# Kernel tuning notes

Measured on AMD Instinct MI355X. Metric: run time of the kernel, lower is better.

## Reference

```python
import jax, jax.numpy as jnp
import numpy as np

SEQ_LEN = 4096
DIM_HALF = 2048  # x last dim = 2 * DIM_HALF
DIM_OUT = 1024
LN_EPS = 1e-5


def setup_inputs() -> dict:
    key = jax.random.key(0)
    k1, k2, k3 = jax.random.split(key, 3)
    x = jax.random.normal(k1, (SEQ_LEN, 2 * DIM_HALF), dtype=jnp.float32)
    ln_scale = jnp.ones((DIM_HALF,), dtype=jnp.float32)
    # original init is uniform(-eps/n, eps/n); scale randn similarly small
    spatial_weights = jax.random.normal(k2, (SEQ_LEN, SEQ_LEN), dtype=jnp.float32) * (0.001 / SEQ_LEN)
    spatial_biases = jnp.ones((SEQ_LEN, 1), dtype=jnp.float32)
    proj_w = jax.random.normal(k3, (DIM_HALF, DIM_OUT), dtype=jnp.float32) * (1.0 / np.sqrt(DIM_HALF))
    proj_b = jnp.zeros((DIM_OUT,), dtype=jnp.float32)
    return {"x": x, "ln_scale": ln_scale, "spatial_weights": spatial_weights,
            "spatial_biases": spatial_biases, "proj_w": proj_w, "proj_b": proj_b}


def reference(x, ln_scale, spatial_weights, spatial_biases, proj_w, proj_b):
    # split into value half and gate half
    xh, gate = jnp.split(x, 2, axis=-1)  # each (n, d)
    # LayerNorm (scale only, no offset), haiku default eps=1e-5
    mean = jnp.mean(gate, axis=-1, keepdims=True)
    var = jnp.var(gate, axis=-1, keepdims=True)
    gate = (gate - mean) * jax.lax.rsqrt(var + LN_EPS) * ln_scale
    # causal (lower-triangular) masked spatial mixing: out[m,d] = sum_n w[m,n] * gate[n,d]
    n = spatial_weights.shape[0]
    w = jnp.tril(spatial_weights)
    gate = jnp.einsum('nd,mn->md', gate, w) + spatial_biases  # (n, d)
    # gating multiply + output projection
    out = (xh * gate) @ proj_w + proj_b  # (n, dim_out)
    return out
```

## Files before the change

kernel.cpp:

```cpp
#include <hip/hip_runtime.h>
#include <cstdint>
#include <cstddef>

#define SEQ 4096
#define DH 2048
#define DOUT 1024

typedef float f32x4 __attribute__((ext_vector_type(4)));
typedef __bf16 bf16x8 __attribute__((ext_vector_type(8)));


__device__ __forceinline__ unsigned short f2bf(float f) {
  unsigned int u = __float_as_uint(f);
  unsigned int r = (u + 0x7FFFu + ((u >> 16) & 1u)) >> 16;
  return (unsigned short)r;
}

__device__ __forceinline__ void g2l16(const unsigned short* g, unsigned short* l) {
  __builtin_amdgcn_global_load_lds((__attribute__((address_space(1))) void*)(void*)g,
                                   (__attribute__((address_space(3))) void*)l, 16, 0, 0);
}


__global__ __launch_bounds__(256) void ln_stats(const float* __restrict__ x,
                                                float* __restrict__ mv,
                                                float* __restrict__ rv) {
  int row = blockIdx.x;
  const float4* g4 = (const float4*)(x + (size_t)row * (2 * DH) + DH);
  float4 a = g4[threadIdx.x];
  float4 b = g4[threadIdx.x + 256];
  float s  = a.x + a.y + a.z + a.w + b.x + b.y + b.z + b.w;
  float s2 = a.x * a.x + a.y * a.y + a.z * a.z + a.w * a.w +
             b.x * b.x + b.y * b.y + b.z * b.z + b.w * b.w;
#pragma unroll
  for (int o = 32; o > 0; o >>= 1) {
    s  += __shfl_down(s, o);
    s2 += __shfl_down(s2, o);
  }
  __shared__ float red[8];
  int wave = threadIdx.x >> 6;
  if ((threadIdx.x & 63) == 0) { red[wave] = s; red[wave + 4] = s2; }
  __syncthreads();
  if (threadIdx.x == 0) {
    float S  = red[0] + red[1] + red[2] + red[3];
    float S2 = red[4] + red[5] + red[6] + red[7];
    float mean = S * (1.0f / DH);
    float var  = S2 * (1.0f / DH) - mean * mean;
    mv[row] = mean;
    rv[row] = rsqrtf(var + 1e-5f);
  }
}


__global__ __launch_bounds__(256) void norm_tr(const float* __restrict__ x,
                                               const float* __restrict__ mv,
                                               const float* __restrict__ rv,
                                               const float* __restrict__ lns,
                                               unsigned short* __restrict__ gateT) {
  __shared__ float tile[64][65];
  int d0 = blockIdx.x * 64;
  int n0 = blockIdx.y * 64;
#pragma unroll
  for (int i = 0; i < 16; i++) {
    int idx = threadIdx.x + i * 256;
    int r = idx >> 6, c = idx & 63;
    float v = x[(size_t)(n0 + r) * (2 * DH) + DH + d0 + c];
    tile[r][c] = (v - mv[n0 + r]) * rv[n0 + r];
  }
  __syncthreads();
#pragma unroll
  for (int i = 0; i < 16; i++) {
    int idx = threadIdx.x + i * 256;
    int dr = idx >> 6, nc = idx & 63;
    float v = tile[nc][dr] * lns[d0 + dr];
    gateT[(size_t)(d0 + dr) * SEQ + n0 + nc] = f2bf(v);
  }
}


__global__ __launch_bounds__(256) void cast_w_tril(const float* __restrict__ w,
                                                   unsigned short* __restrict__ wb) {
  size_t e = ((size_t)blockIdx.x * 256 + threadIdx.x) * 8;
  int m = (int)(e >> 12);
  int k = (int)(e & 4095);
  uint4 o;
  if (k + 7 <= m) {
    const float4* s = (const float4*)(w + e);
    float4 a = s[0], b = s[1];
    o.x = (unsigned)f2bf(a.x) | ((unsigned)f2bf(a.y) << 16);
    o.y = (unsigned)f2bf(a.z) | ((unsigned)f2bf(a.w) << 16);
    o.z = (unsigned)f2bf(b.x) | ((unsigned)f2bf(b.y) << 16);
    o.w = (unsigned)f2bf(b.z) | ((unsigned)f2bf(b.w) << 16);
  } else if (k > m) {
    o.x = o.y = o.z = o.w = 0u;
  } else {
    unsigned short t[8];
#pragma unroll
    for (int j = 0; j < 8; j++) t[j] = (k + j <= m) ? f2bf(w[e + j]) : (unsigned short)0;
    o.x = (unsigned)t[0] | ((unsigned)t[1] << 16);
    o.y = (unsigned)t[2] | ((unsigned)t[3] << 16);
    o.z = (unsigned)t[4] | ((unsigned)t[5] << 16);
    o.w = (unsigned)t[6] | ((unsigned)t[7] << 16);
  }
  *(uint4*)(wb + e) = o;
}


__global__ __launch_bounds__(256) void proj_tr(const float* __restrict__ pw,
                                               unsigned short* __restrict__ pT) {
  __shared__ float tile[64][65];
  int j0 = blockIdx.x * 64;
  int d0 = blockIdx.y * 64;
#pragma unroll
  for (int i = 0; i < 16; i++) {
    int idx = threadIdx.x + i * 256;
    int r = idx >> 6, c = idx & 63;
    tile[r][c] = pw[(size_t)(d0 + r) * DOUT + j0 + c];
  }
  __syncthreads();
#pragma unroll
  for (int i = 0; i < 16; i++) {
    int idx = threadIdx.x + i * 256;
    int jr = idx >> 6, dc = idx & 63;
    pT[(size_t)(j0 + jr) * DH + d0 + dc] = f2bf(tile[dc][jr]);
  }
}


template <bool PAIR, int EPI>
__global__ __launch_bounds__(256) void gemm64(const unsigned short* __restrict__ A,
                                              const unsigned short* __restrict__ BT,
                                              const float* __restrict__ xfull,
                                              const float* __restrict__ rbias,
                                              unsigned short* __restrict__ Pout,
                                              const float* __restrict__ cbias,
                                              float* __restrict__ out,
                                              int N, int K) {
  constexpr int BM = 64, BN = 64, BK = 64;
  __shared__ unsigned short sA[BM * BK];
  __shared__ unsigned short sB[BN * BK];

  const int tid = threadIdx.x;
  const int lane = tid & 63, wave = tid >> 6;
  const int quad = lane >> 4, l16 = lane & 15;
  const int wm = wave >> 1, wn = wave & 1;
  const int bn0 = blockIdx.x * BN;

  int sRow[2], sCol[2];
#pragma unroll
  for (int r = 0; r < 2; r++) {
    int idx = r * 256 + tid;
    int row = idx >> 3;
    sRow[r] = row;
    sCol[r] = ((idx & 7) ^ (row & 7)) * 8;
  }

  const int nTiles = PAIR ? 2 : 1;
  for (int t = 0; t < nTiles; t++) {
    const int by = PAIR ? (t == 0 ? (int)blockIdx.y : (2 * (int)gridDim.y - 1 - (int)blockIdx.y))
                        : (int)blockIdx.y;
    const int bm0 = by * BM;
    const int kEnd = PAIR ? (bm0 + BM) : K;

    const unsigned short* aSrc[2];
    const unsigned short* bSrc[2];
    unsigned short* aDst[2];
    unsigned short* bDst[2];
#pragma unroll
    for (int r = 0; r < 2; r++) {
      aSrc[r] = A + (size_t)(bm0 + sRow[r]) * K + sCol[r];
      bSrc[r] = BT + (size_t)(bn0 + sRow[r]) * K + sCol[r];
      aDst[r] = &sA[(size_t)(r * 256 + tid) * 8];
      bDst[r] = &sB[(size_t)(r * 256 + tid) * 8];
    }

    f32x4 acc[2][2] = {};

    for (int k0 = 0; k0 < kEnd; k0 += BK) {
#pragma unroll
      for (int r = 0; r < 2; r++) { g2l16(aSrc[r], aDst[r]); aSrc[r] += BK; }
#pragma unroll
      for (int r = 0; r < 2; r++) { g2l16(bSrc[r], bDst[r]); bSrc[r] += BK; }
      __syncthreads();

      bf16x8 af[2][2], bf[2][2];
#pragma unroll
      for (int h = 0; h < 2; h++) {
#pragma unroll
        for (int i = 0; i < 2; i++) {
          int R = wm * 32 + i * 16 + l16;
          af[h][i] = *(const bf16x8*)&sA[R * BK + (((h * 4 + quad) ^ (R & 7)) * 8)];
        }
#pragma unroll
        for (int j = 0; j < 2; j++) {
          int R = wn * 32 + j * 16 + l16;
          bf[h][j] = *(const bf16x8*)&sB[R * BK + (((h * 4 + quad) ^ (R & 7)) * 8)];
        }
      }
#pragma unroll
      for (int h = 0; h < 2; h++)
#pragma unroll
        for (int i = 0; i < 2; i++)
#pragma unroll
          for (int j = 0; j < 2; j++)
            acc[i][j] = __builtin_amdgcn_mfma_f32_16x16x32_bf16(af[h][i], bf[h][j], acc[i][j], 0, 0, 0);
      __syncthreads();
    }

#pragma unroll
    for (int i = 0; i < 2; i++) {
#pragma unroll
      for (int j = 0; j < 2; j++) {
        int col = bn0 + wn * 32 + j * 16 + l16;
#pragma unroll
        for (int r = 0; r < 4; r++) {
          int row = bm0 + wm * 32 + i * 16 + quad * 4 + r;
          float v = acc[i][j][r];
          if (EPI == 1) {
            float g = v + rbias[row];
            float pv = xfull[(size_t)row * (2 * DH) + col] * g;
            Pout[(size_t)row * N + col] = f2bf(pv);
          } else {
            out[(size_t)row * N + col] = v + cbias[col];
          }
        }
      }
    }
    if (PAIR && t == 0) __syncthreads();
  }
}


extern "C" void kernel_launch(void* const* d_in, const int* in_sizes, int n_in,
                              void* d_out, int out_size, void* d_ws, size_t ws_size,
                              hipStream_t stream) {
  (void)in_sizes; (void)n_in; (void)out_size; (void)ws_size;
  const float* x   = (const float*)d_in[0];
  const float* lns = (const float*)d_in[1];
  const float* w   = (const float*)d_in[2];
  const float* sb  = (const float*)d_in[3];
  const float* pw  = (const float*)d_in[4];
  const float* pb  = (const float*)d_in[5];
  float* out = (float*)d_out;

  char* p = (char*)d_ws;
  unsigned short* gateT = (unsigned short*)p; p += (size_t)DH * SEQ * 2;
  unsigned short* wb    = (unsigned short*)p; p += (size_t)SEQ * SEQ * 2;
  unsigned short* projT = (unsigned short*)p; p += (size_t)DOUT * DH * 2;
  unsigned short* Pbuf  = (unsigned short*)p; p += (size_t)SEQ * DH * 2;
  float* mv = (float*)p; p += (size_t)SEQ * 4;
  float* rv = (float*)p; p += (size_t)SEQ * 4;

  ln_stats<<<SEQ, 256, 0, stream>>>(x, mv, rv);
  norm_tr<<<dim3(DH / 64, SEQ / 64), 256, 0, stream>>>(x, mv, rv, lns, gateT);
  cast_w_tril<<<(int)(((size_t)SEQ * SEQ / 8) / 256), 256, 0, stream>>>(w, wb);
  proj_tr<<<dim3(DOUT / 64, DH / 64), 256, 0, stream>>>(pw, projT);

  gemm64<true, 1><<<dim3(DH / 64, SEQ / 128), 256, 0, stream>>>(
      wb, gateT, x, sb, Pbuf, nullptr, nullptr, DH, SEQ);
  gemm64<false, 2><<<dim3(DOUT / 64, SEQ / 64), 256, 0, stream>>>(
      Pbuf, projT, nullptr, nullptr, nullptr, pb, out, DOUT, DH);
}
```

Before: 255.3 us.

## Use 128x128 double-buffered GEMM tiles with fused causal tile-pair loop

Both GEMMs move from 64x64 tiles to 128x128 tiles, so each wave now computes a 64x64 sub-block with 16 MFMA accumulators. This raises operand reuse per LDS load. The LDS buffers are doubled so the next K-slice is loaded into one buffer while the current one is being computed. The two causal tiles of the spatial GEMM now run as one continuous pipelined loop, with the first tile's epilogue placed mid-loop. The costs are more registers and LDS, one block per CU, and fewer blocks in the grid.

```diff
diff --git a/kernel.cpp b/kernel.cpp
--- a/kernel.cpp
+++ b/kernel.cpp
@@ -128,93 +128,86 @@
 
 
 template <bool PAIR, int EPI>
-__global__ __launch_bounds__(256) void gemm64(const unsigned short* __restrict__ A,
-                                              const unsigned short* __restrict__ BT,
-                                              const float* __restrict__ xfull,
-                                              const float* __restrict__ rbias,
-                                              unsigned short* __restrict__ Pout,
-                                              const float* __restrict__ cbias,
-                                              float* __restrict__ out,
-                                              int N, int K) {
-  constexpr int BM = 64, BN = 64, BK = 64;
-  __shared__ unsigned short sA[BM * BK];
-  __shared__ unsigned short sB[BN * BK];
+__global__ __launch_bounds__(256, 1) void gemm128(const unsigned short* __restrict__ A,
+                                                  const unsigned short* __restrict__ BT,
+                                                  const float* __restrict__ xfull,
+                                                  const float* __restrict__ rbias,
+                                                  unsigned short* __restrict__ Pout,
+                                                  const float* __restrict__ cbias,
+                                                  float* __restrict__ out,
+                                                  int N, int K) {
+  constexpr int BK = 64;
+  __shared__ unsigned short sA[2][128 * BK];
+  __shared__ unsigned short sB[2][128 * BK];
 
   const int tid = threadIdx.x;
   const int lane = tid & 63, wave = tid >> 6;
   const int quad = lane >> 4, l16 = lane & 15;
   const int wm = wave >> 1, wn = wave & 1;
-  const int bn0 = blockIdx.x * BN;
-
-  int sRow[2], sCol[2];
-#pragma unroll
-  for (int r = 0; r < 2; r++) {
+  const int bn0 = blockIdx.x * 128;
+  const int p = blockIdx.y;
+
+  const int bm0a = p * 128;
+  const int bm0b = PAIR ? (2 * (int)gridDim.y - 1 - p) * 128 : 0;
+  const int e1 = PAIR ? 2 * (p + 1) : (K / BK);
+  const int total = PAIR ? (2 + 4 * (int)gridDim.y) : (K / BK);
+
+  int sOff[4], sDst[4];
+#pragma unroll
+  for (int r = 0; r < 4; r++) {
     int idx = r * 256 + tid;
     int row = idx >> 3;
-    sRow[r] = row;
-    sCol[r] = ((idx & 7) ^ (row & 7)) * 8;
-  }
-
-  const int nTiles = PAIR ? 2 : 1;
-  for (int t = 0; t < nTiles; t++) {
-    const int by = PAIR ? (t == 0 ? (int)blockIdx.y : (2 * (int)gridDim.y - 1 - (int)blockIdx.y))
-                        : (int)blockIdx.y;
-    const int bm0 = by * BM;
-    const int kEnd = PAIR ? (bm0 + BM) : K;
-
-    const unsigned short* aSrc[2];
-    const unsigned short* bSrc[2];
-    unsigned short* aDst[2];
-    unsigned short* bDst[2];
-#pragma unroll
-    for (int r = 0; r < 2; r++) {
-      aSrc[r] = A + (size_t)(bm0 + sRow[r]) * K + sCol[r];
-      bSrc[r] = BT + (size_t)(bn0 + sRow[r]) * K + sCol[r];
-      aDst[r] = &sA[(size_t)(r * 256 + tid) * 8];
-      bDst[r] = &sB[(size_t)(r * 256 + tid) * 8];
+    sOff[r] = row * K + (((idx & 7) ^ (row & 7)) * 8);
+    sDst[r] = idx * 8;
+  }
+
+  f32x4 acc[4][4] = {};
+
+  auto stage = [&](int i, int b) {
+    int kk, bm;
+    if (!PAIR || i < e1) { kk = i * BK; bm = bm0a; }
+    else                 { kk = (i - e1) * BK; bm = bm0b; }
+    const unsigned short* Ab = A + (size_t)bm * K + kk;
+    const unsigned short* Bb = BT + (size_t)bn0 * K + kk;
+#pragma unroll
+    for (int r = 0; r < 4; r++) g2l16(Ab + sOff[r], &sA[b][sDst[r]]);
+#pragma unroll
+    for (int r = 0; r < 4; r++) g2l16(Bb + sOff[r], &sB[b][sDst[r]]);
+  };
+
+  auto compute = [&](int b) {
+    bf16x8 af[2][4], bf[2][4];
+#pragma unroll
+    for (int h = 0; h < 2; h++) {
+#pragma unroll
+      for (int i = 0; i < 4; i++) {
+        int R = wm * 64 + i * 16 + l16;
+        af[h][i] = *(const bf16x8*)&sA[b][R * BK + (((h * 4 + quad) ^ (R & 7)) * 8)];
+      }
+#pragma unroll
+      for (int j = 0; j < 4; j++) {
+        int R = wn * 64 + j * 16 + l16;
+        bf[h][j] = *(const bf16x8*)&sB[b][R * BK + (((h * 4 + quad) ^ (R & 7)) * 8)];
+      }
     }
-
-    f32x4 acc[2][2] = {};
-
-    for (int k0 = 0; k0 < kEnd; k0 += BK) {
-#pragma unroll
-      for (int r = 0; r < 2; r++) { g2l16(aSrc[r], aDst[r]); aSrc[r] += BK; }
-#pragma unroll
-      for (int r = 0; r < 2; r++) { g2l16(bSrc[r], bDst[r]); bSrc[r] += BK; }
-      __syncthreads();
-
-      bf16x8 af[2][2], bf[2][2];
-#pragma unroll
-      for (int h = 0; h < 2; h++) {
-#pragma unroll
-        for (int i = 0; i < 2; i++) {
-          int R = wm * 32 + i * 16 + l16;
-          af[h][i] = *(const bf16x8*)&sA[R * BK + (((h * 4 + quad) ^ (R & 7)) * 8)];
-        }
-#pragma unroll
-        for (int j = 0; j < 2; j++) {
-          int R = wn * 32 + j * 16 + l16;
-          bf[h][j] = *(const bf16x8*)&sB[R * BK + (((h * 4 + quad) ^ (R & 7)) * 8)];
-        }
-      }
-#pragma unroll
-      for (int h = 0; h < 2; h++)
-#pragma unroll
-        for (int i = 0; i < 2; i++)
-#pragma unroll
-          for (int j = 0; j < 2; j++)
-            acc[i][j] = __builtin_amdgcn_mfma_f32_16x16x32_bf16(af[h][i], bf[h][j], acc[i][j], 0, 0, 0);
-      __syncthreads();
-    }
-
-#pragma unroll
-    for (int i = 0; i < 2; i++) {
-#pragma unroll
-      for (int j = 0; j < 2; j++) {
-        int col = bn0 + wn * 32 + j * 16 + l16;
+#pragma unroll
+    for (int h = 0; h < 2; h++)
+#pragma unroll
+      for (int i = 0; i < 4; i++)
+#pragma unroll
+        for (int j = 0; j < 4; j++)
+          acc[i][j] = __builtin_amdgcn_mfma_f32_16x16x32_bf16(af[h][i], bf[h][j], acc[i][j], 0, 0, 0);
+  };
+
+  auto epilogue = [&](int bm0) {
+#pragma unroll
+    for (int i = 0; i < 4; i++) {
+#pragma unroll
+      for (int j = 0; j < 4; j++) {
+        int col = bn0 + wn * 64 + j * 16 + l16;
 #pragma unroll
         for (int r = 0; r < 4; r++) {
-          int row = bm0 + wm * 32 + i * 16 + quad * 4 + r;
+          int row = bm0 + wm * 64 + i * 16 + quad * 4 + r;
           float v = acc[i][j][r];
           if (EPI == 1) {
             float g = v + rbias[row];
@@ -226,8 +219,23 @@
         }
       }
     }
-    if (PAIR && t == 0) __syncthreads();
-  }
+  };
+
+  stage(0, 0);
+  __syncthreads();
+  for (int i = 0; i < total; i++) {
+    if (i + 1 < total) stage(i + 1, (i + 1) & 1);
+    compute(i & 1);
+    if (PAIR && i == e1 - 1) {
+      epilogue(bm0a);
+#pragma unroll
+      for (int a = 0; a < 4; a++)
+#pragma unroll
+        for (int bj = 0; bj < 4; bj++) acc[a][bj] = (f32x4){0.f, 0.f, 0.f, 0.f};
+    }
+    __syncthreads();
+  }
+  epilogue(PAIR ? bm0b : bm0a);
 }
 
 
@@ -256,8 +264,8 @@
   cast_w_tril<<<(int)(((size_t)SEQ * SEQ / 8) / 256), 256, 0, stream>>>(w, wb);
   proj_tr<<<dim3(DOUT / 64, DH / 64), 256, 0, stream>>>(pw, projT);
 
-  gemm64<true, 1><<<dim3(DH / 64, SEQ / 128), 256, 0, stream>>>(
+  gemm128<true, 1><<<dim3(DH / 128, SEQ / 256), 256, 0, stream>>>(
       wb, gateT, x, sb, Pbuf, nullptr, nullptr, DH, SEQ);
-  gemm64<false, 2><<<dim3(DOUT / 64, SEQ / 64), 256, 0, stream>>>(
+  gemm128<false, 2><<<dim3(DOUT / 128, SEQ / 128), 256, 0, stream>>>(
       Pbuf, projT, nullptr, nullptr, nullptr, pb, out, DOUT, DH);
 }
```

After: 304.6 us. 1.19x slower.

## Enlarge GEMM block tile to 128x64 with four-row-fragment waves

Applied to the files above, without the earlier changes.

Both GEMMs now use a 128x64 output tile per 256-thread block instead of 64x64, so each wave computes a 64x32 sub-tile from four A fragments and two B fragments. This raises MFMA work per LDS load and per global byte, and halves the block count. It also drops the extra barrier between the paired causal tiles. In exchange it uses more registers and LDS per block and leaves fewer blocks to fill the CUs, which may lower occupancy.

```diff
diff --git a/kernel.cpp b/kernel.cpp
--- a/kernel.cpp
+++ b/kernel.cpp
@@ -128,67 +128,58 @@
 
 
 template <bool PAIR, int EPI>
-__global__ __launch_bounds__(256) void gemm64(const unsigned short* __restrict__ A,
-                                              const unsigned short* __restrict__ BT,
-                                              const float* __restrict__ xfull,
-                                              const float* __restrict__ rbias,
-                                              unsigned short* __restrict__ Pout,
-                                              const float* __restrict__ cbias,
-                                              float* __restrict__ out,
-                                              int N, int K) {
-  constexpr int BM = 64, BN = 64, BK = 64;
-  __shared__ unsigned short sA[BM * BK];
-  __shared__ unsigned short sB[BN * BK];
+__global__ __launch_bounds__(256) void gemm12864(const unsigned short* __restrict__ A,
+                                                 const unsigned short* __restrict__ BT,
+                                                 const float* __restrict__ xfull,
+                                                 const float* __restrict__ rbias,
+                                                 unsigned short* __restrict__ Pout,
+                                                 const float* __restrict__ cbias,
+                                                 float* __restrict__ out,
+                                                 int N, int K) {
+  constexpr int BK = 64;
+  __shared__ unsigned short sA[128 * BK];
+  __shared__ unsigned short sB[64 * BK];
 
   const int tid = threadIdx.x;
   const int lane = tid & 63, wave = tid >> 6;
   const int quad = lane >> 4, l16 = lane & 15;
   const int wm = wave >> 1, wn = wave & 1;
-  const int bn0 = blockIdx.x * BN;
-
-  int sRow[2], sCol[2];
-#pragma unroll
-  for (int r = 0; r < 2; r++) {
+  const int bn0 = blockIdx.x * 64;
+  const int p = blockIdx.y;
+
+  int sOff[4], sDst[4];
+#pragma unroll
+  for (int r = 0; r < 4; r++) {
     int idx = r * 256 + tid;
     int row = idx >> 3;
-    sRow[r] = row;
-    sCol[r] = ((idx & 7) ^ (row & 7)) * 8;
+    sOff[r] = row * K + (((idx & 7) ^ (row & 7)) * 8);
+    sDst[r] = idx * 8;
   }
 
   const int nTiles = PAIR ? 2 : 1;
   for (int t = 0; t < nTiles; t++) {
-    const int by = PAIR ? (t == 0 ? (int)blockIdx.y : (2 * (int)gridDim.y - 1 - (int)blockIdx.y))
-                        : (int)blockIdx.y;
-    const int bm0 = by * BM;
-    const int kEnd = PAIR ? (bm0 + BM) : K;
-
-    const unsigned short* aSrc[2];
-    const unsigned short* bSrc[2];
-    unsigned short* aDst[2];
-    unsigned short* bDst[2];
-#pragma unroll
-    for (int r = 0; r < 2; r++) {
-      aSrc[r] = A + (size_t)(bm0 + sRow[r]) * K + sCol[r];
-      bSrc[r] = BT + (size_t)(bn0 + sRow[r]) * K + sCol[r];
-      aDst[r] = &sA[(size_t)(r * 256 + tid) * 8];
-      bDst[r] = &sB[(size_t)(r * 256 + tid) * 8];
-    }
-
-    f32x4 acc[2][2] = {};
+    const int by = PAIR ? (t == 0 ? p : (2 * (int)gridDim.y - 1 - p)) : p;
+    const int bm0 = by * 128;
+    const int kEnd = PAIR ? (bm0 + 128) : K;
+
+    const unsigned short* Ab = A + (size_t)bm0 * K;
+    const unsigned short* Bb = BT + (size_t)bn0 * K;
+
+    f32x4 acc[4][2] = {};
 
     for (int k0 = 0; k0 < kEnd; k0 += BK) {
 #pragma unroll
-      for (int r = 0; r < 2; r++) { g2l16(aSrc[r], aDst[r]); aSrc[r] += BK; }
-#pragma unroll
-      for (int r = 0; r < 2; r++) { g2l16(bSrc[r], bDst[r]); bSrc[r] += BK; }
+      for (int r = 0; r < 4; r++) g2l16(Ab + k0 + sOff[r], &sA[sDst[r]]);
+#pragma unroll
+      for (int r = 0; r < 2; r++) g2l16(Bb + k0 + sOff[r], &sB[sDst[r]]);
       __syncthreads();
 
-      bf16x8 af[2][2], bf[2][2];
+      bf16x8 af[2][4], bf[2][2];
 #pragma unroll
       for (int h = 0; h < 2; h++) {
 #pragma unroll
-        for (int i = 0; i < 2; i++) {
-          int R = wm * 32 + i * 16 + l16;
+        for (int i = 0; i < 4; i++) {
+          int R = wm * 64 + i * 16 + l16;
           af[h][i] = *(const bf16x8*)&sA[R * BK + (((h * 4 + quad) ^ (R & 7)) * 8)];
         }
 #pragma unroll
@@ -200,7 +191,7 @@
 #pragma unroll
       for (int h = 0; h < 2; h++)
 #pragma unroll
-        for (int i = 0; i < 2; i++)
+        for (int i = 0; i < 4; i++)
 #pragma unroll
           for (int j = 0; j < 2; j++)
             acc[i][j] = __builtin_amdgcn_mfma_f32_16x16x32_bf16(af[h][i], bf[h][j], acc[i][j], 0, 0, 0);
@@ -208,13 +199,13 @@
     }
 
 #pragma unroll
-    for (int i = 0; i < 2; i++) {
+    for (int i = 0; i < 4; i++) {
 #pragma unroll
       for (int j = 0; j < 2; j++) {
         int col = bn0 + wn * 32 + j * 16 + l16;
 #pragma unroll
         for (int r = 0; r < 4; r++) {
-          int row = bm0 + wm * 32 + i * 16 + quad * 4 + r;
+          int row = bm0 + wm * 64 + i * 16 + quad * 4 + r;
           float v = acc[i][j][r];
           if (EPI == 1) {
             float g = v + rbias[row];
@@ -226,7 +217,6 @@
         }
       }
     }
-    if (PAIR && t == 0) __syncthreads();
   }
 }
 
@@ -256,8 +246,8 @@
   cast_w_tril<<<(int)(((size_t)SEQ * SEQ / 8) / 256), 256, 0, stream>>>(w, wb);
   proj_tr<<<dim3(DOUT / 64, DH / 64), 256, 0, stream>>>(pw, projT);
 
-  gemm64<true, 1><<<dim3(DH / 64, SEQ / 128), 256, 0, stream>>>(
+  gemm12864<true, 1><<<dim3(DH / 64, SEQ / 256), 256, 0, stream>>>(
       wb, gateT, x, sb, Pbuf, nullptr, nullptr, DH, SEQ);
-  gemm64<false, 2><<<dim3(DOUT / 64, SEQ / 64), 256, 0, stream>>>(
+  gemm12864<false, 2><<<dim3(DOUT / 64, SEQ / 128), 256, 0, stream>>>(
       Pbuf, projT, nullptr, nullptr, nullptr, pb, out, DOUT, DH);
 }
```

Result: slower. 270.2 us (+5.8%).
